# Kernel tuning notes

Measured on AMD Instinct MI355X. Metric: run time of the kernel, lower is better.

## Reference

```python
import jax, jax.numpy as jnp
import numpy as np

B, L, D_MODEL = 2, 2048, 1024
HEADS, DH, K = 8, 128, 64  # d_head = d_model // heads, kernel_width window
DILATIONS = np.array([1, 1, 2, 2, 4, 4, 8, 8], dtype=np.int32)  # per-head dilation


def setup_inputs() -> dict:
    key = jax.random.key(0)
    ks = jax.random.split(key, 8)
    s_in = 1.0 / np.sqrt(D_MODEL)       # kaiming-uniform-ish fan_in bound
    s_c = 1.0 / np.sqrt(HEADS * DH)
    return {
        "query": jax.random.normal(ks[0], (B, L, D_MODEL), dtype=jnp.float32),
        "key": jax.random.normal(ks[1], (B, L, D_MODEL), dtype=jnp.float32),
        "value": jax.random.normal(ks[2], (B, L, D_MODEL), dtype=jnp.float32),
        "Wq": jax.random.uniform(ks[3], (HEADS, DH, D_MODEL), minval=-s_in, maxval=s_in),
        "bq": jnp.zeros((HEADS, DH), dtype=jnp.float32),
        "Wk": jax.random.uniform(ks[4], (HEADS, DH, D_MODEL), minval=-s_in, maxval=s_in),
        "bk": jnp.zeros((HEADS, DH), dtype=jnp.float32),
        "Wv": jax.random.uniform(ks[5], (HEADS, DH, D_MODEL), minval=-s_in, maxval=s_in),
        "bv": jnp.zeros((HEADS, DH), dtype=jnp.float32),
        "Wc": jax.random.uniform(ks[6], (D_MODEL, HEADS * DH), minval=-s_c, maxval=s_c),
        "bc": jnp.zeros((D_MODEL,), dtype=jnp.float32),
    }


def reference(query, key, value, Wq, bq, Wk, bk, Wv, bv, Wc, bc):
    Lq = query.shape[-2]
    # per-head linear projections: [B,L,D] x [H,DH,D] -> [B,H,L,DH]
    q = jnp.einsum('bld,hed->bhle', query, Wq) + bq[:, None, :]
    k = jnp.einsum('bld,hed->bhle', key, Wk) + bk[:, None, :]
    v = jnp.einsum('bld,hed->bhle', value, Wv) + bv[:, None, :]

    # dilated, centered local windows (per-head dilation)
    offsets = jnp.arange(K) - (K - 1) // 2                     # [K]
    dil = jnp.asarray(DILATIONS)                               # [H]
    idx = (jnp.arange(Lq)[None, :, None]
           + offsets[None, None, :] * dil[:, None, None])      # [H, L, K]
    valid = (idx >= 0) & (idx < Lq)
    idxc = jnp.clip(idx, 0, Lq - 1)

    # gather per-head windows: x [B,H,L,DH], idx [H,L,K] -> [B,H,L,K,DH]
    gather = jax.vmap(lambda xh, ih: xh[:, ih], in_axes=(1, 0), out_axes=1)
    k_win = gather(k, idxc)
    v_win = gather(v, idxc)

    # banded attention (original applies no 1/sqrt(d) scaling)
    scores = jnp.einsum('bhld,bhlkd->bhlk', q, k_win)
    scores = jnp.where(valid[None], scores, jnp.asarray(-1e9, scores.dtype))
    attn = jax.nn.softmax(scores, axis=-1)
    out = jnp.einsum('bhlk,bhlkd->bhld', attn, v_win)

    # merge heads and collapse back to d_model
    out = out.transpose(0, 2, 1, 3).reshape(out.shape[0], Lq, HEADS * DH)
    return out @ Wc.T + bc
```

## Files before the change

### kernel.cpp

```cpp
#include <hip/hip_runtime.h>
#include <hip/hip_bf16.h>
#include <stdint.h>

#define NB 2
#define LQ 2048
#define DMODEL 1024
#define NH 8
#define DH 128
#define KWIN 64

typedef __attribute__((ext_vector_type(8))) short short8;
typedef __attribute__((ext_vector_type(4))) float f32x4;

__device__ __forceinline__ ushort f2bf(float f) {
  uint u = __float_as_uint(f);
  return (ushort)((u + 0x7fffu + ((u >> 16) & 1u)) >> 16);
}
__device__ __forceinline__ float bflo(uint u) { return __uint_as_float(u << 16); }
__device__ __forceinline__ float bfhi(uint u) { return __uint_as_float(u & 0xffff0000u); }

__global__ void cvt_qkv(const float4* __restrict__ a, const float4* __restrict__ b,
                        const float4* __restrict__ c, ushort* __restrict__ da,
                        ushort* __restrict__ db, ushort* __restrict__ dc, int n4) {
  int stride = gridDim.x * blockDim.x;
  for (int i = blockIdx.x * blockDim.x + threadIdx.x; i < n4; i += stride) {
    float4 x = a[i], y = b[i], z = c[i];
    *(ushort4*)(da + 4 * (size_t)i) = make_ushort4(f2bf(x.x), f2bf(x.y), f2bf(x.z), f2bf(x.w));
    *(ushort4*)(db + 4 * (size_t)i) = make_ushort4(f2bf(y.x), f2bf(y.y), f2bf(y.z), f2bf(y.w));
    *(ushort4*)(dc + 4 * (size_t)i) = make_ushort4(f2bf(z.x), f2bf(z.y), f2bf(z.z), f2bf(z.w));
  }
}

__global__ void cvt_w(const float4* __restrict__ a, const float4* __restrict__ b,
                      const float4* __restrict__ c, const float4* __restrict__ d,
                      ushort* __restrict__ da, ushort* __restrict__ db,
                      ushort* __restrict__ dc, ushort* __restrict__ dd, int n4) {
  int stride = gridDim.x * blockDim.x;
  for (int i = blockIdx.x * blockDim.x + threadIdx.x; i < n4; i += stride) {
    float4 x = a[i], y = b[i], z = c[i], w = d[i];
    *(ushort4*)(da + 4 * (size_t)i) = make_ushort4(f2bf(x.x), f2bf(x.y), f2bf(x.z), f2bf(x.w));
    *(ushort4*)(db + 4 * (size_t)i) = make_ushort4(f2bf(y.x), f2bf(y.y), f2bf(y.z), f2bf(y.w));
    *(ushort4*)(dc + 4 * (size_t)i) = make_ushort4(f2bf(z.x), f2bf(z.y), f2bf(z.z), f2bf(z.w));
    *(ushort4*)(dd + 4 * (size_t)i) = make_ushort4(f2bf(w.x), f2bf(w.y), f2bf(w.z), f2bf(w.w));
  }
}

template <int OUT_BF16>
__global__ __launch_bounds__(256, 4) void gemm_bt(
    const ushort* __restrict__ A0, const ushort* __restrict__ B0,
    const float* __restrict__ c0, void* __restrict__ D0,
    const ushort* __restrict__ A1, const ushort* __restrict__ B1,
    const float* __restrict__ c1, void* __restrict__ D1,
    const ushort* __restrict__ A2, const ushort* __restrict__ B2,
    const float* __restrict__ c2, void* __restrict__ D2,
    int M, int N, int Kd) {
  const int gx = gridDim.x, gy = gridDim.y;
  const int nblk = gx * gy * gridDim.z;
  const int fid = (blockIdx.z * gy + blockIdx.y) * gx + blockIdx.x;
  const int cpx = nblk >> 3;
  const int nid = (fid & 7) * cpx + (fid >> 3);
  const int z = nid / (gx * gy);
  const int rem = nid % (gx * gy);
  const int m0 = (rem / gx) * 128;
  const int n0 = (rem % gx) * 128;

  const ushort* A = (z == 0) ? A0 : ((z == 1) ? A1 : A2);
  const ushort* Bt = (z == 0) ? B0 : ((z == 1) ? B1 : B2);
  const float* bias = (z == 0) ? c0 : ((z == 1) ? c1 : c2);
  void* Cv = (z == 0) ? D0 : ((z == 1) ? D1 : D2);

  __shared__ ushort As[2][128 * 32];
  __shared__ ushort Bs[2][128 * 32];

  const int tid = threadIdx.x;
  const int wave = tid >> 6, lane = tid & 63;
  const int wm = wave >> 1, wn = wave & 1;
  const int lrow = lane & 15, kgrp = lane >> 4;

  const int b0 = tid * 16;
  const int b1 = b0 + 4096;
  const int r0 = b0 >> 6, cc0 = (b0 & 63) >> 1;
  const int r1 = b1 >> 6, cc1 = (b1 & 63) >> 1;

  const ushort* gA0 = A + (size_t)(m0 + r0) * Kd + cc0;
  const ushort* gA1 = A + (size_t)(m0 + r1) * Kd + cc1;
  const ushort* gB0 = Bt + (size_t)(n0 + r0) * Kd + cc0;
  const ushort* gB1 = Bt + (size_t)(n0 + r1) * Kd + cc1;

  auto stage = [&](int buf, int kt) {
    __builtin_amdgcn_global_load_lds(
        (const __attribute__((address_space(1))) void*)(gA0 + kt),
        (__attribute__((address_space(3))) void*)(As[buf] + (b0 >> 1)), 16, 0, 0);
    __builtin_amdgcn_global_load_lds(
        (const __attribute__((address_space(1))) void*)(gA1 + kt),
        (__attribute__((address_space(3))) void*)(As[buf] + (b1 >> 1)), 16, 0, 0);
    __builtin_amdgcn_global_load_lds(
        (const __attribute__((address_space(1))) void*)(gB0 + kt),
        (__attribute__((address_space(3))) void*)(Bs[buf] + (b0 >> 1)), 16, 0, 0);
    __builtin_amdgcn_global_load_lds(
        (const __attribute__((address_space(1))) void*)(gB1 + kt),
        (__attribute__((address_space(3))) void*)(Bs[buf] + (b1 >> 1)), 16, 0, 0);
  };

  f32x4 acc[4][4] = {};

  auto compute = [&](int buf) {
    short8 af[4], bfr[4];
#pragma unroll
    for (int m = 0; m < 4; ++m)
      af[m] = *(const short8*)(As[buf] + (wm * 64 + m * 16 + lrow) * 32 + kgrp * 8);
#pragma unroll
    for (int n = 0; n < 4; ++n)
      bfr[n] = *(const short8*)(Bs[buf] + (wn * 64 + n * 16 + lrow) * 32 + kgrp * 8);
#pragma unroll
    for (int m = 0; m < 4; ++m)
#pragma unroll
      for (int n = 0; n < 4; ++n)
        acc[m][n] = __builtin_amdgcn_mfma_f32_16x16x32_bf16(af[m], bfr[n], acc[m][n], 0, 0, 0);
  };

  const int nt = Kd >> 5;
  stage(0, 0);
  __syncthreads();
  int cur = 0;
  for (int it = 0; it < nt - 1; ++it) {
    stage(cur ^ 1, (it + 1) << 5);
    compute(cur);
    __syncthreads();
    cur ^= 1;
  }
  compute(cur);

  const int cbase = n0 + wn * 64;
  const int rbase = m0 + wm * 64;
  float bv[4];
#pragma unroll
  for (int n = 0; n < 4; ++n) bv[n] = bias[cbase + n * 16 + lrow];

#pragma unroll
  for (int m = 0; m < 4; ++m) {
#pragma unroll
    for (int n = 0; n < 4; ++n) {
      const int col = cbase + n * 16 + lrow;
#pragma unroll
      for (int j = 0; j < 4; ++j) {
        const int row = rbase + m * 16 + kgrp * 4 + j;
        float val = acc[m][n][j] + bv[n];
        if (OUT_BF16) {
          ((ushort*)Cv)[(size_t)row * N + col] = f2bf(val);
        } else {
          ((float*)Cv)[(size_t)row * N + col] = val;
        }
      }
    }
  }
}

__global__ __launch_bounds__(128) void banded_attn_mfma(
    const ushort* __restrict__ qp, const ushort* __restrict__ kp,
    const ushort* __restrict__ vp, ushort* __restrict__ ao) {
  __shared__ ushort Qs[32 * 128];
  __shared__ ushort Ks[96 * 128];
  __shared__ ushort Vs[112 * 128];
  __shared__ ushort Ps[2][16 * 104];
  __shared__ ushort Os[2][16 * 128];

  const int tid = threadIdx.x;
  const int wv = tid >> 6;
  const int lane = tid & 63;
  const int lrow = lane & 15, kgrp = lane >> 4;

  const int blk = blockIdx.x;
  const int chunk = blk & 63;
  const int h = (blk >> 6) & 7;
  const int b = blk >> 9;
  const int sh = h >> 1;
  const int dil = 1 << sh;
  const int Ld = LQ >> sh;
  const int rres = chunk >> (6 - sh);
  const int tile = chunk & ((64 >> sh) - 1);
  const int t0 = tile << 5;
  const int p0 = t0 - 32;

  const size_t headoff = (size_t)h * DH;
  const size_t bbase = (size_t)b * LQ * (NH * DH);

  const int srow = lane >> 4;
  const int sc = lane & 15;
  for (int it = wv; it < 60; it += 2) {
    int rbase, pstart;
    const ushort* g;
    ushort* ld;
    if (it < 8) {
      rbase = it * 4; pstart = t0; g = qp; ld = Qs;
    } else if (it < 32) {
      rbase = (it - 8) * 4; pstart = p0; g = kp; ld = Ks;
    } else {
      rbase = (it - 32) * 4; pstart = p0; g = vp; ld = Vs;
    }
    int row = rbase + srow;
    int key = (row ^ (row >> 3)) & 7;
    int cs = sc ^ key;
    int t = pstart + row;
    t = t < 0 ? 0 : (t >= Ld ? Ld - 1 : t);
    int l = rres + t * dil;
    const ushort* src = g + bbase + (size_t)l * (NH * DH) + headoff + cs * 8;
    __builtin_amdgcn_global_load_lds(
        (const __attribute__((address_space(1))) void*)src,
        (__attribute__((address_space(3))) void*)(ld + rbase * 128), 16, 0, 0);
  }
  __syncthreads();

  const int iblk = wv << 4;
  f32x4 accs[5] = {};
#pragma unroll
  for (int ks = 0; ks < 4; ++ks) {
    const int qrow = iblk + lrow;
    const int qslot = (ks * 4 + kgrp) ^ ((qrow ^ (qrow >> 3)) & 7);
    short8 qf = *(const short8*)(Qs + qrow * 128 + qslot * 8);
#pragma unroll
    for (int t = 0; t < 5; ++t) {
      const int krow = (wv + t) * 16 + lrow;
      const int kslot = (ks * 4 + kgrp) ^ ((krow ^ (krow >> 3)) & 7);
      short8 kf = *(const short8*)(Ks + krow * 128 + kslot * 8);
      accs[t] = __builtin_amdgcn_mfma_f32_16x16x32_bf16(qf, kf, accs[t], 0, 0, 0);
    }
  }

  float dens[4];
#pragma unroll
  for (int j = 0; j < 4; ++j) {
    const int i_b = iblk + kgrp * 4 + j;
    float mj = -1e30f;
#pragma unroll
    for (int t = 0; t < 5; ++t) {
      const int jj = (wv + t) * 16 + lrow;
      const int p = p0 + jj;
      const bool ok = (jj >= i_b + 1) && (jj <= i_b + 64) && (p >= 0) && (p < Ld);
      float v = ok ? accs[t][j] : -1e30f;
      accs[t][j] = v;
      mj = fmaxf(mj, v);
    }
#pragma unroll
    for (int off = 1; off < 16; off <<= 1) mj = fmaxf(mj, __shfl_xor(mj, off));
    float dj = 0.f;
#pragma unroll
    for (int t = 0; t < 5; ++t) {
      float e = __expf(accs[t][j] - mj);
      accs[t][j] = e;
      dj += e;
    }
#pragma unroll
    for (int off = 1; off < 16; off <<= 1) dj += __shfl_xor(dj, off);
    dens[j] = dj;
  }

  ushort* Pw = Ps[wv];
#pragma unroll
  for (int j = 0; j < 4; ++j) {
    const int prow = kgrp * 4 + j;
#pragma unroll
    for (int t = 0; t < 5; ++t) Pw[prow * 104 + t * 16 + lrow] = f2bf(accs[t][j]);
    Pw[prow * 104 + 80 + lrow] = 0;
  }

  f32x4 accv[8] = {};
#pragma unroll
  for (int ks = 0; ks < 3; ++ks) {
    short8 pf = *(const short8*)(Pw + lrow * 104 + ks * 32 + kgrp * 8);
#pragma unroll
    for (int dt = 0; dt < 8; ++dt) {
      short8 vf;
#pragma unroll
      for (int rr = 0; rr < 8; ++rr) {
        const int vrow = iblk + ks * 32 + kgrp * 8 + rr;
        const int d = dt * 16 + lrow;
        const int slot = (d >> 3) ^ ((vrow ^ (vrow >> 3)) & 7);
        vf[rr] = (short)Vs[vrow * 128 + slot * 8 + (d & 7)];
      }
      accv[dt] = __builtin_amdgcn_mfma_f32_16x16x32_bf16(pf, vf, accv[dt], 0, 0, 0);
    }
  }

  ushort* Ow = Os[wv];
#pragma unroll
  for (int j = 0; j < 4; ++j) {
    const float inv = 1.f / dens[j];
    const int orow = kgrp * 4 + j;
#pragma unroll
    for (int dt = 0; dt < 8; ++dt)
      Ow[orow * 128 + dt * 16 + lrow] = f2bf(accv[dt][j] * inv);
  }
#pragma unroll
  for (int pass = 0; pass < 4; ++pass) {
    const int i_loc = pass * 4 + srow;
    const int tq = t0 + iblk + i_loc;
    const int l = rres + tq * dil;
    short8 vvv = *(const short8*)(Ow + i_loc * 128 + sc * 8);
    *(short8*)(ao + bbase + (size_t)l * (NH * DH) + headoff + sc * 8) = vvv;
  }
}

extern "C" void kernel_launch(void* const* d_in, const int* in_sizes, int n_in,
                              void* d_out, int out_size, void* d_ws, size_t ws_size,
                              hipStream_t stream) {
  const float* q = (const float*)d_in[0];
  const float* k = (const float*)d_in[1];
  const float* v = (const float*)d_in[2];
  const float* Wq = (const float*)d_in[3];
  const float* bq = (const float*)d_in[4];
  const float* Wk = (const float*)d_in[5];
  const float* bk = (const float*)d_in[6];
  const float* Wv = (const float*)d_in[7];
  const float* bv = (const float*)d_in[8];
  const float* Wc = (const float*)d_in[9];
  const float* bc = (const float*)d_in[10];

  const size_t NIN = (size_t)NB * LQ * DMODEL;
  const size_t NW = (size_t)NH * DH * DMODEL;

  ushort* qin = (ushort*)d_ws;
  ushort* kin = qin + NIN;
  ushort* vin = kin + NIN;
  ushort* wqb = vin + NIN;
  ushort* wkb = wqb + NW;
  ushort* wvb = wkb + NW;
  ushort* wcb = wvb + NW;
  ushort* qp = wcb + NW;
  ushort* kp = qp + NIN;
  ushort* vp = kp + NIN;
  ushort* aob = vp + NIN;

  hipLaunchKernelGGL(cvt_qkv, dim3(2048), dim3(256), 0, stream,
                     (const float4*)q, (const float4*)k, (const float4*)v,
                     qin, kin, vin, (int)(NIN / 4));
  hipLaunchKernelGGL(cvt_w, dim3(1024), dim3(256), 0, stream,
                     (const float4*)Wq, (const float4*)Wk, (const float4*)Wv, (const float4*)Wc,
                     wqb, wkb, wvb, wcb, (int)(NW / 4));

  dim3 g1(DMODEL / 128, (NB * LQ) / 128, 3);
  hipLaunchKernelGGL((gemm_bt<1>), g1, dim3(256), 0, stream,
                     qin, wqb, bq, (void*)qp,
                     kin, wkb, bk, (void*)kp,
                     vin, wvb, bv, (void*)vp,
                     NB * LQ, DMODEL, DMODEL);

  hipLaunchKernelGGL(banded_attn_mfma, dim3(NB * NH * 64), dim3(128), 0, stream,
                     qp, kp, vp, aob);

  dim3 g2(DMODEL / 128, (NB * LQ) / 128, 1);
  hipLaunchKernelGGL((gemm_bt<0>), g2, dim3(256), 0, stream,
                     aob, wcb, bc, d_out,
                     aob, wcb, bc, d_out,
                     aob, wcb, bc, d_out,
                     NB * LQ, DMODEL, DMODEL);
}
```

Measured before the change: 101.1 us.

## Use 256x256 tiled QKV GEMM with 4-stage direct-to-LDS pipeline and merged conversion kernel

Replaces the 128x128 QKV projection GEMM with a 512-thread 256x256 tile kernel. Operands are loaded straight into LDS with global_load_lds across a 4-slot ring and 3 tiles of prefetch, gated by explicit vmcnt waits. The two fp32-to-bf16 conversion kernels are merged into one launch over a contiguous workspace, and the output GEMM becomes its own fp32-output kernel. The aim is more data reuse per tile, better hiding of load latency, and one fewer launch. The trade-offs are a 192-block grid that may underfill the GPU, higher register pressure from 8x4 accumulators, and 128KB of LDS per block.

```diff
diff --git a/kernel.cpp b/kernel.cpp
--- a/kernel.cpp
+++ b/kernel.cpp
@@ -19,40 +19,39 @@
 __device__ __forceinline__ float bflo(uint u) { return __uint_as_float(u << 16); }
 __device__ __forceinline__ float bfhi(uint u) { return __uint_as_float(u & 0xffff0000u); }
 
-__global__ void cvt_qkv(const float4* __restrict__ a, const float4* __restrict__ b,
-                        const float4* __restrict__ c, ushort* __restrict__ da,
-                        ushort* __restrict__ db, ushort* __restrict__ dc, int n4) {
-  int stride = gridDim.x * blockDim.x;
-  for (int i = blockIdx.x * blockDim.x + threadIdx.x; i < n4; i += stride) {
-    float4 x = a[i], y = b[i], z = c[i];
-    *(ushort4*)(da + 4 * (size_t)i) = make_ushort4(f2bf(x.x), f2bf(x.y), f2bf(x.z), f2bf(x.w));
-    *(ushort4*)(db + 4 * (size_t)i) = make_ushort4(f2bf(y.x), f2bf(y.y), f2bf(y.z), f2bf(y.w));
-    *(ushort4*)(dc + 4 * (size_t)i) = make_ushort4(f2bf(z.x), f2bf(z.y), f2bf(z.z), f2bf(z.w));
-  }
-}
-
-__global__ void cvt_w(const float4* __restrict__ a, const float4* __restrict__ b,
-                      const float4* __restrict__ c, const float4* __restrict__ d,
-                      ushort* __restrict__ da, ushort* __restrict__ db,
-                      ushort* __restrict__ dc, ushort* __restrict__ dd, int n4) {
-  int stride = gridDim.x * blockDim.x;
-  for (int i = blockIdx.x * blockDim.x + threadIdx.x; i < n4; i += stride) {
-    float4 x = a[i], y = b[i], z = c[i], w = d[i];
-    *(ushort4*)(da + 4 * (size_t)i) = make_ushort4(f2bf(x.x), f2bf(x.y), f2bf(x.z), f2bf(x.w));
-    *(ushort4*)(db + 4 * (size_t)i) = make_ushort4(f2bf(y.x), f2bf(y.y), f2bf(y.z), f2bf(y.w));
-    *(ushort4*)(dc + 4 * (size_t)i) = make_ushort4(f2bf(z.x), f2bf(z.y), f2bf(z.z), f2bf(z.w));
-    *(ushort4*)(dd + 4 * (size_t)i) = make_ushort4(f2bf(w.x), f2bf(w.y), f2bf(w.z), f2bf(w.w));
-  }
-}
-
-template <int OUT_BF16>
-__global__ __launch_bounds__(256, 4) void gemm_bt(
+__global__ void cvt_all(const float4* __restrict__ q, const float4* __restrict__ k,
+                        const float4* __restrict__ v, const float4* __restrict__ wq,
+                        const float4* __restrict__ wk, const float4* __restrict__ wv,
+                        const float4* __restrict__ wc, ushort4* __restrict__ dst) {
+  const int n4in = (NB * LQ * DMODEL) / 4;
+  const int n4w = (NH * DH * DMODEL) / 4;
+  const int total = 3 * n4in + 4 * n4w;
+  const int stride = gridDim.x * blockDim.x;
+  for (int i = blockIdx.x * blockDim.x + threadIdx.x; i < total; i += stride) {
+    const float4* src;
+    int off;
+    if (i < 3 * n4in) {
+      const int r = i >> 20;
+      off = i & (n4in - 1);
+      src = (r == 0) ? q : ((r == 1) ? k : v);
+    } else {
+      const int j = i - 3 * n4in;
+      const int r = j >> 18;
+      off = j & (n4w - 1);
+      src = (r == 0) ? wq : ((r == 1) ? wk : ((r == 2) ? wv : wc));
+    }
+    float4 x = src[off];
+    dst[i] = make_ushort4(f2bf(x.x), f2bf(x.y), f2bf(x.z), f2bf(x.w));
+  }
+}
+
+__global__ __launch_bounds__(512, 2) void gemm256_qkv(
     const ushort* __restrict__ A0, const ushort* __restrict__ B0,
-    const float* __restrict__ c0, void* __restrict__ D0,
+    const float* __restrict__ c0, ushort* __restrict__ D0,
     const ushort* __restrict__ A1, const ushort* __restrict__ B1,
-    const float* __restrict__ c1, void* __restrict__ D1,
+    const float* __restrict__ c1, ushort* __restrict__ D1,
     const ushort* __restrict__ A2, const ushort* __restrict__ B2,
-    const float* __restrict__ c2, void* __restrict__ D2,
+    const float* __restrict__ c2, ushort* __restrict__ D2,
     int M, int N, int Kd) {
   const int gx = gridDim.x, gy = gridDim.y;
   const int nblk = gx * gy * gridDim.z;
@@ -61,13 +60,118 @@
   const int nid = (fid & 7) * cpx + (fid >> 3);
   const int z = nid / (gx * gy);
   const int rem = nid % (gx * gy);
-  const int m0 = (rem / gx) * 128;
-  const int n0 = (rem % gx) * 128;
+  const int m0 = (rem / gx) * 256;
+  const int n0 = (rem % gx) * 256;
 
   const ushort* A = (z == 0) ? A0 : ((z == 1) ? A1 : A2);
   const ushort* Bt = (z == 0) ? B0 : ((z == 1) ? B1 : B2);
   const float* bias = (z == 0) ? c0 : ((z == 1) ? c1 : c2);
-  void* Cv = (z == 0) ? D0 : ((z == 1) ? D1 : D2);
+  ushort* Cv = (z == 0) ? D0 : ((z == 1) ? D1 : D2);
+
+  __shared__ ushort LDS[4 * 16384];
+
+  const int tid = threadIdx.x;
+  const int wave = tid >> 6, lane = tid & 63;
+  const int wm = wave >> 2, wn = wave & 3;
+  const int lrow = lane & 15, kgrp = lane >> 4;
+
+  const int b = tid * 16;
+  const int srow = b >> 6;
+  const int scc = (b & 63) >> 1;
+
+  const ushort* gA0 = A + (size_t)(m0 + srow) * Kd + scc;
+  const ushort* gA1 = A + (size_t)(m0 + 128 + srow) * Kd + scc;
+  const ushort* gB0 = Bt + (size_t)(n0 + srow) * Kd + scc;
+  const ushort* gB1 = Bt + (size_t)(n0 + 128 + srow) * Kd + scc;
+  const int dso = b >> 1;
+
+  auto STAGE = [&](int slot, int kt) {
+    ushort* sl = LDS + slot * 16384;
+    __builtin_amdgcn_global_load_lds(
+        (const __attribute__((address_space(1))) void*)(gA0 + kt),
+        (__attribute__((address_space(3))) void*)(sl + dso), 16, 0, 0);
+    __builtin_amdgcn_global_load_lds(
+        (const __attribute__((address_space(1))) void*)(gA1 + kt),
+        (__attribute__((address_space(3))) void*)(sl + 4096 + dso), 16, 0, 0);
+    __builtin_amdgcn_global_load_lds(
+        (const __attribute__((address_space(1))) void*)(gB0 + kt),
+        (__attribute__((address_space(3))) void*)(sl + 8192 + dso), 16, 0, 0);
+    __builtin_amdgcn_global_load_lds(
+        (const __attribute__((address_space(1))) void*)(gB1 + kt),
+        (__attribute__((address_space(3))) void*)(sl + 12288 + dso), 16, 0, 0);
+  };
+
+  f32x4 acc[8][4] = {};
+  const int NT = Kd >> 5;
+
+  STAGE(0, 0);
+  STAGE(1, 32);
+  STAGE(2, 64);
+
+  for (int t = 0; t < NT; ++t) {
+    const int pf = t + 3;
+    if (pf < NT) {
+      STAGE(pf & 3, pf << 5);
+      asm volatile("s_waitcnt vmcnt(12)" ::: "memory");
+    } else if (pf == NT) {
+      asm volatile("s_waitcnt vmcnt(8)" ::: "memory");
+    } else if (pf == NT + 1) {
+      asm volatile("s_waitcnt vmcnt(4)" ::: "memory");
+    } else {
+      asm volatile("s_waitcnt vmcnt(0)" ::: "memory");
+    }
+    __builtin_amdgcn_s_barrier();
+    __builtin_amdgcn_sched_barrier(0);
+
+    const ushort* sA = LDS + (t & 3) * 16384 + wm * 4096 + lrow * 32 + kgrp * 8;
+    const ushort* sB = LDS + (t & 3) * 16384 + 8192 + (wn >> 1) * 4096 +
+                       ((wn & 1) * 64 + lrow) * 32 + kgrp * 8;
+    short8 af[8], bfr[4];
+#pragma unroll
+    for (int m = 0; m < 8; ++m) af[m] = *(const short8*)(sA + m * 512);
+#pragma unroll
+    for (int n = 0; n < 4; ++n) bfr[n] = *(const short8*)(sB + n * 512);
+    asm volatile("s_waitcnt lgkmcnt(0)" ::: "memory");
+    __builtin_amdgcn_sched_barrier(0);
+    __builtin_amdgcn_s_barrier();
+
+#pragma unroll
+    for (int m = 0; m < 8; ++m)
+#pragma unroll
+      for (int n = 0; n < 4; ++n)
+        acc[m][n] = __builtin_amdgcn_mfma_f32_16x16x32_bf16(af[m], bfr[n], acc[m][n], 0, 0, 0);
+  }
+
+  const int cbase = n0 + wn * 64;
+  const int rbase = m0 + wm * 128;
+  float bv[4];
+#pragma unroll
+  for (int n = 0; n < 4; ++n) bv[n] = bias[cbase + n * 16 + lrow];
+
+#pragma unroll
+  for (int m = 0; m < 8; ++m) {
+#pragma unroll
+    for (int n = 0; n < 4; ++n) {
+      const int col = cbase + n * 16 + lrow;
+#pragma unroll
+      for (int j = 0; j < 4; ++j) {
+        const int row = rbase + m * 16 + kgrp * 4 + j;
+        Cv[(size_t)row * N + col] = f2bf(acc[m][n][j] + bv[n]);
+      }
+    }
+  }
+}
+
+__global__ __launch_bounds__(256, 4) void gemm_out(
+    const ushort* __restrict__ A, const ushort* __restrict__ Bt,
+    const float* __restrict__ bias, float* __restrict__ Cv, int M, int N, int Kd) {
+  const int gx = gridDim.x, gy = gridDim.y;
+  const int nblk = gx * gy;
+  const int fid = blockIdx.y * gx + blockIdx.x;
+  const int cpx = nblk >> 3;
+  const int nid = (fid & 7) * cpx + (fid >> 3);
+  const int m0 = (nid / gx) * 128;
+  const int n0 = (nid % gx) * 128;
 
   __shared__ ushort As[2][128 * 32];
   __shared__ ushort Bs[2][128 * 32];
@@ -145,12 +249,7 @@
 #pragma unroll
       for (int j = 0; j < 4; ++j) {
         const int row = rbase + m * 16 + kgrp * 4 + j;
-        float val = acc[m][n][j] + bv[n];
-        if (OUT_BF16) {
-          ((ushort*)Cv)[(size_t)row * N + col] = f2bf(val);
-        } else {
-          ((float*)Cv)[(size_t)row * N + col] = val;
-        }
+        Cv[(size_t)row * N + col] = acc[m][n][j] + bv[n];
       }
     }
   }
@@ -331,27 +430,22 @@
   ushort* vp = kp + NIN;
   ushort* aob = vp + NIN;
 
-  hipLaunchKernelGGL(cvt_qkv, dim3(2048), dim3(256), 0, stream,
+  hipLaunchKernelGGL(cvt_all, dim3(2048), dim3(256), 0, stream,
                      (const float4*)q, (const float4*)k, (const float4*)v,
-                     qin, kin, vin, (int)(NIN / 4));
-  hipLaunchKernelGGL(cvt_w, dim3(1024), dim3(256), 0, stream,
-                     (const float4*)Wq, (const float4*)Wk, (const float4*)Wv, (const float4*)Wc,
-                     wqb, wkb, wvb, wcb, (int)(NW / 4));
-
-  dim3 g1(DMODEL / 128, (NB * LQ) / 128, 3);
-  hipLaunchKernelGGL((gemm_bt<1>), g1, dim3(256), 0, stream,
-                     qin, wqb, bq, (void*)qp,
-                     kin, wkb, bk, (void*)kp,
-                     vin, wvb, bv, (void*)vp,
+                     (const float4*)Wq, (const float4*)Wk, (const float4*)Wv,
+                     (const float4*)Wc, (ushort4*)qin);
+
+  dim3 g1(DMODEL / 256, (NB * LQ) / 256, 3);
+  hipLaunchKernelGGL(gemm256_qkv, g1, dim3(512), 0, stream,
+                     qin, wqb, bq, qp,
+                     kin, wkb, bk, kp,
+                     vin, wvb, bv, vp,
                      NB * LQ, DMODEL, DMODEL);
 
   hipLaunchKernelGGL(banded_attn_mfma, dim3(NB * NH * 64), dim3(128), 0, stream,
                      qp, kp, vp, aob);
 
-  dim3 g2(DMODEL / 128, (NB * LQ) / 128, 1);
-  hipLaunchKernelGGL((gemm_bt<0>), g2, dim3(256), 0, stream,
-                     aob, wcb, bc, d_out,
-                     aob, wcb, bc, d_out,
-                     aob, wcb, bc, d_out,
-                     NB * LQ, DMODEL, DMODEL);
-}
+  dim3 g2(DMODEL / 128, (NB * LQ) / 128);
+  hipLaunchKernelGGL(gemm_out, g2, dim3(256), 0, stream,
+                     aob, wcb, bc, (float*)d_out, NB * LQ, DMODEL, DMODEL);
+}
```

Result: slower. 104.0 us (+2.8%).
